# Kernel tuning notes

Measured on AMD Instinct MI355X. Metric: run time of the kernel, lower is better.

## Reference

```python
import jax, jax.numpy as jnp
import numpy as np

RADIUS = 1.3
COARSE = 64
FINE = 2
N_ATOMS = 64
SH_DIM = 9
DATA_DIM = SH_DIM * 3 + 1  # 28
N_INTRS = COARSE * 3 * 2 * FINE  # 768
STEP = (RADIUS * 2.0 / COARSE / FINE) / 2.0
BATCH = 1024


def sh_basis(d):
    # real spherical harmonics basis, degree 2 (9 coeffs), on normalized dirs
    d = d / jnp.linalg.norm(d, axis=-1, keepdims=True)
    x, y, z = d[..., 0], d[..., 1], d[..., 2]
    C0 = 0.28209479177387814
    C1 = 0.4886025119029199
    C20, C21, C22, C23, C24 = (1.0925484305920792, -1.0925484305920792,
                               0.31539156525252005, -1.0925484305920792,
                               0.5462742152960396)
    return jnp.stack([
        C0 * jnp.ones_like(x), -C1 * y, C1 * z, -C1 * x,
        C20 * x * y, C21 * y * z, C22 * (2.0 * z * z - x * x - y * y),
        C23 * x * z, C24 * (x * x - y * y)
    ], axis=-1)


def dict_interp(grid, atoms, pts):
    # l2_interp_v2: coarse-voxel dictionary coeffs x trilinear fine-atom interp
    # pts: [P,3] in [0,1)
    P = pts.shape[0]
    pc = pts * COARSE
    c = jnp.clip(jnp.floor(pc), 0, COARSE - 1).astype(jnp.int32)
    local = pc - c.astype(pts.dtype)  # position inside coarse voxel, [0,1)
    clin = (c[:, 0] * COARSE + c[:, 1]) * COARSE + c[:, 2]
    coeff = grid[clin]                              # [P, A]
    # project dictionary coeffs through atoms for every fine cell: [P, FINE^3, D]
    proj = jnp.einsum('pa,fad->pfd', coeff, atoms)
    u = local * FINE - 0.5
    f = jnp.floor(u)
    t = u - f
    i0 = jnp.clip(f, 0, FINE - 1).astype(jnp.int32)
    i1 = jnp.clip(f + 1.0, 0, FINE - 1).astype(jnp.int32)
    idx = jnp.stack([i0, i1], axis=-1)              # [P,3,2]
    w = jnp.stack([1.0 - t, t], axis=-1)            # [P,3,2]
    rows = jnp.arange(P)
    out = jnp.zeros((P, DATA_DIM), dtype=pts.dtype)
    for kx in (0, 1):
        for ky in (0, 1):
            for kz in (0, 1):
                lin = (idx[:, 0, kx] * FINE + idx[:, 1, ky]) * FINE + idx[:, 2, kz]
                wgt = w[:, 0, kx] * w[:, 1, ky] * w[:, 2, kz]
                out = out + wgt[:, None] * proj[rows, lin]
    return out


def _forward(rays_o, rays_d, grid, atoms):
    dt = rays_o.dtype
    # ---- sample_proposal (no grad) ----
    off_pos = (RADIUS - rays_o) / rays_d
    off_neg = (-RADIUS - rays_o) / rays_d
    start = jnp.max(jnp.minimum(off_pos, off_neg), axis=-1, keepdims=True)
    intersections = jax.lax.stop_gradient(
        start + jnp.arange(N_INTRS, dtype=dt)[None, :] * STEP)  # [B, 768]
    tr = intersections[:, :-1]  # [B, 767]
    pts = rays_o[:, None, :] + tr[..., None] * rays_d[:, None, :]  # [B,n,3]
    mask = jnp.all((pts > -RADIUS) & (pts < RADIUS), axis=-1)      # [B,n]
    pts = jax.lax.stop_gradient(pts)
    B, n = tr.shape
    # normalized coords in [0,1); masked-out points are clipped then zeroed later
    p = jnp.clip((pts + RADIUS) / (2.0 * RADIUS), 0.0, 1.0 - 1e-6).reshape(-1, 3)
    data = dict_interp(grid, atoms, p).reshape(B, n, DATA_DIM)
    # masked_scatter of sigma <=> dense compute + where(mask, ., 0)
    sigma = jnp.where(mask, jax.nn.relu(data[..., -1]), 0.0)
    dists = (intersections[:, 1:] - intersections[:, :-1]) * \
        jnp.linalg.norm(rays_d, axis=-1, keepdims=True)
    alpha = 1.0 - jnp.exp(-sigma * dists)
    trans = jnp.cumprod(1.0 - alpha + 1e-10, axis=-1)
    trans = jnp.concatenate([jnp.ones_like(trans[:, :1]), trans[:, :-1]], axis=-1)
    abs_light = alpha * trans  # per-sample weights
    sh_mult = sh_basis(rays_d)                      # [B, 9]
    sh = data[..., :-1].reshape(B, n, 3, SH_DIM)
    rgb_samp = jnp.einsum('bnck,bk->bnc', sh, sh_mult)
    rgb_samp = jax.nn.sigmoid(jnp.where(mask[..., None], rgb_samp, 0.0))
    comp = jnp.sum(abs_light[..., None] * rgb_samp, axis=1)  # [B,3]
    acc = jnp.sum(abs_light, axis=1)
    rgb = comp + (1.0 - acc)[:, None]  # white background
    depth = jnp.sum(abs_light * tr, axis=1)
    return rgb, alpha, depth


def setup_inputs():
    key = jax.random.key(0)
    k0, k1, k2, k3 = jax.random.split(key, 4)
    o = jax.random.normal(k0, (BATCH, 3), dtype=jnp.float32)
    o = o / jnp.linalg.norm(o, axis=-1, keepdims=True) * 2.5
    d = -o + 0.3 * jax.random.normal(k1, (BATCH, 3), dtype=jnp.float32)
    d = d / jnp.linalg.norm(d, axis=-1, keepdims=True)
    grid = 0.01 * jax.random.normal(k2, (COARSE ** 3, N_ATOMS), dtype=jnp.float32)
    atoms_sh = jax.random.uniform(k3, (FINE ** 3, N_ATOMS, DATA_DIM - 1), dtype=jnp.float32)
    atoms = jnp.concatenate(
        [atoms_sh, jnp.full((FINE ** 3, N_ATOMS, 1), 0.01, dtype=jnp.float32)], axis=-1)
    return {"rays_o": o, "rays_d": d, "grid": grid, "atoms": atoms, "grid_id": 0}


def reference(rays_o, rays_d, grid, atoms, grid_id):
    # grid_id selects among num_scenes grids; num_scenes=1 so grid is pre-selected
    return _forward(rays_o, rays_d, grid, atoms)
```

## Files before the change

### kernel.cpp

```cpp
#include <hip/hip_runtime.h>
#include <hip/hip_bf16.h>

#define RADIUS_F 1.3f
#define NSAMP 767
#define STEPF 0.01015625f
#define BATCH 1024

typedef __attribute__((ext_vector_type(8))) short short8;
typedef __attribute__((ext_vector_type(4))) float floatx4;

static __device__ __forceinline__ unsigned pkbf(float a, float b) {
    union { __hip_bfloat162 h; unsigned u; } cvt;
    cvt.h = __float22bfloat162_rn(make_float2(a, b));
    return cvt.u;
}

static __device__ __forceinline__ float coset4_sum(float p) {
    int q4 = __builtin_amdgcn_update_dpp(0, __float_as_int(p), 0x124, 0xf, 0xf, true);
    p = p + __int_as_float(q4);
    int q8 = __builtin_amdgcn_update_dpp(0, __float_as_int(p), 0x128, 0xf, 0xf, true);
    return p + __int_as_float(q8);
}

__launch_bounds__(256, 2)
__global__ void plenoxels_fwd(const float* __restrict__ rays_o,
                              const float* __restrict__ rays_d,
                              const float* __restrict__ grid,
                              const float* __restrict__ atoms,
                              float* __restrict__ out)
{
    __shared__ __align__(16) __hip_bfloat16 BpL[32 * 64];
    __shared__ __align__(16) float WL[4][16 * 12];
    __shared__ __align__(16) __hip_bfloat16 alphaL[768];
    __shared__ __align__(16) __hip_bfloat16 rgbL[768 * 3];

    const int tid  = threadIdx.x;
    const int ray  = blockIdx.x;
    const int lane = tid & 63;
    const int w    = tid >> 6;
    const int m    = lane & 15;
    const int quad = lane >> 4;

    const float ox = rays_o[ray * 3 + 0], oy = rays_o[ray * 3 + 1], oz = rays_o[ray * 3 + 2];
    const float dx = rays_d[ray * 3 + 0], dy = rays_d[ray * 3 + 1], dz = rays_d[ray * 3 + 2];

    float start;
    {
        float a0 = (RADIUS_F - ox) / dx, b0 = (-RADIUS_F - ox) / dx;
        float a1 = (RADIUS_F - oy) / dy, b1 = (-RADIUS_F - oy) / dy;
        float a2 = (RADIUS_F - oz) / dz, b2 = (-RADIUS_F - oz) / dz;
        start = fmaxf(fminf(a0, b0), fmaxf(fminf(a1, b1), fminf(a2, b2)));
    }
    const float dnorm = sqrtf(dx * dx + dy * dy + dz * dz);
    const float dist = STEPF * dnorm;

    float shm[9];
    {
        float inv = 1.0f / dnorm;
        float nx = dx * inv, ny = dy * inv, nz = dz * inv;
        shm[0] = 0.28209479177387814f;
        shm[1] = -0.4886025119029199f * ny;
        shm[2] = 0.4886025119029199f * nz;
        shm[3] = -0.4886025119029199f * nx;
        shm[4] = 1.0925484305920792f * nx * ny;
        shm[5] = -1.0925484305920792f * ny * nz;
        shm[6] = 0.31539156525252005f * (2.f * nz * nz - nx * nx - ny * ny);
        shm[7] = -1.0925484305920792f * nx * nz;
        shm[8] = 0.5462742152960396f * (nx * nx - ny * ny);
    }

    for (int idx = tid; idx < 2048; idx += 256) {
        int col = idx >> 6, a = idx & 63;
        int f = col >> 2, c = col & 3;
        const float* base = atoms + (f * 64 + a) * 28;
        float sv;
        if (c == 3) sv = base[27];
        else {
            sv = 0.f;
            #pragma unroll
            for (int i = 0; i < 9; ++i) sv = fmaf(base[c * 9 + i], shm[i], sv);
        }
        BpL[col * 64 + a] = __float2bfloat16(sv);
    }
    __syncthreads();

    short8 bq00, bq01, bq10, bq11;
    {
        const short* bs = (const short*)BpL;
        const short* p0 = bs + m * 64 + (quad << 4);
        bq00 = *(const short8*)(p0);
        bq01 = *(const short8*)(p0 + 8);
        const short* p1 = bs + (16 + m) * 64 + (quad << 4);
        bq10 = *(const short8*)(p1);
        bq11 = *(const short8*)(p1 + 8);
    }

    float* out_rgb   = out;
    float* out_alpha = out + BATCH * 3;
    float* out_depth = out + BATCH * 3 + BATCH * NSAMP;
    const float4* g4 = (const float4*)grid;

    auto geom = [&](int s, float4& WA, float4& WB, int& clin) {
        float tr = start + (float)s * STEPF;
        float px = ox + tr * dx, py = oy + tr * dy, pz = oz + tr * dz;
        int mask = (px > -RADIUS_F) & (px < RADIUS_F) &
                   (py > -RADIUS_F) & (py < RADIUS_F) &
                   (pz > -RADIUS_F) & (pz < RADIUS_F);
        float maskf = mask ? 1.f : 0.f;
        const float sc = 1.0f / (2.0f * RADIUS_F);
        float qx = fminf(fmaxf((px + RADIUS_F) * sc, 0.f), 1.0f - 1e-6f);
        float qy = fminf(fmaxf((py + RADIUS_F) * sc, 0.f), 1.0f - 1e-6f);
        float qz = fminf(fmaxf((pz + RADIUS_F) * sc, 0.f), 1.0f - 1e-6f);
        float pcx = qx * 64.f, pcy = qy * 64.f, pcz = qz * 64.f;
        float cx = fminf(floorf(pcx), 63.f);
        float cy = fminf(floorf(pcy), 63.f);
        float cz = fminf(floorf(pcz), 63.f);
        float lx = pcx - cx, ly = pcy - cy, lz = pcz - cz;
        clin = (((int)cx * 64) + (int)cy) * 64 + (int)cz;
        float xw0, xw1, yw0, yw1, zw0, zw1;
        {
            float u = lx * 2.f - 0.5f, fF = floorf(u), t = u - fF;
            xw0 = (fF < 0.f) ? 1.f : ((fF > 0.f) ? 0.f : 1.f - t);
            xw1 = (fF < 0.f) ? 0.f : ((fF > 0.f) ? 1.f : t);
        }
        {
            float u = ly * 2.f - 0.5f, fF = floorf(u), t = u - fF;
            yw0 = (fF < 0.f) ? 1.f : ((fF > 0.f) ? 0.f : 1.f - t);
            yw1 = (fF < 0.f) ? 0.f : ((fF > 0.f) ? 1.f : t);
        }
        {
            float u = lz * 2.f - 0.5f, fF = floorf(u), t = u - fF;
            zw0 = (fF < 0.f) ? 1.f : ((fF > 0.f) ? 0.f : 1.f - t);
            zw1 = (fF < 0.f) ? 0.f : ((fF > 0.f) ? 1.f : t);
        }
        xw0 *= maskf; xw1 *= maskf;
        WA = make_float4(xw0 * yw0 * zw0, xw0 * yw0 * zw1, xw0 * yw1 * zw0, xw0 * yw1 * zw1);
        WB = make_float4(xw1 * yw0 * zw0, xw1 * yw0 * zw1, xw1 * yw1 * zw0, xw1 * yw1 * zw1);
    };

    float4 WAc, WBc; int clinC;
    geom(w * 192 + m, WAc, WBc, clinC);
    float4 cv0, cv1, cv2, cv3;
    {
        const float4* gp = g4 + (clinC << 4) + (quad << 2);
        cv0 = gp[0]; cv1 = gp[1]; cv2 = gp[2]; cv3 = gp[3];
    }

    for (int t = 0; t < 12; ++t) {
        const int tile = w * 12 + t;

        if (quad == 0) {
            float* wrow = &WL[w][m * 12];
            *(float4*)(wrow)     = WAc;
            *(float4*)(wrow + 4) = WBc;
        }

        union { unsigned u[4]; short8 s; } a0, a1;
        a0.u[0] = pkbf(cv0.x, cv0.y); a0.u[1] = pkbf(cv0.z, cv0.w);
        a0.u[2] = pkbf(cv1.x, cv1.y); a0.u[3] = pkbf(cv1.z, cv1.w);
        a1.u[0] = pkbf(cv2.x, cv2.y); a1.u[1] = pkbf(cv2.z, cv2.w);
        a1.u[2] = pkbf(cv3.x, cv3.y); a1.u[3] = pkbf(cv3.z, cv3.w);

        if (t < 11) {
            geom(w * 192 + (t + 1) * 16 + m, WAc, WBc, clinC);
            const float4* gp = g4 + (clinC << 4) + (quad << 2);
            cv0 = gp[0]; cv1 = gp[1]; cv2 = gp[2]; cv3 = gp[3];
        }

        floatx4 acc0 = {0.f, 0.f, 0.f, 0.f};
        floatx4 acc1 = {0.f, 0.f, 0.f, 0.f};
        acc0 = __builtin_amdgcn_mfma_f32_16x16x32_bf16(a0.s, bq00, acc0, 0, 0, 0);
        acc0 = __builtin_amdgcn_mfma_f32_16x16x32_bf16(a1.s, bq01, acc0, 0, 0, 0);
        acc1 = __builtin_amdgcn_mfma_f32_16x16x32_bf16(a0.s, bq10, acc1, 0, 0, 0);
        acc1 = __builtin_amdgcn_mfma_f32_16x16x32_bf16(a1.s, bq11, acc1, 0, 0, 0);

        const int f0 = m >> 2;
        #pragma unroll
        for (int r = 0; r < 4; ++r) {
            const float* wrow = &WL[w][((quad << 2) + r) * 12];
            float wA = wrow[f0];
            float wB = wrow[4 + f0];
            float p = wA * acc0[r] + wB * acc1[r];
            p = coset4_sum(p);
            int s = (tile << 4) + (quad << 2) + r;
            if (s < NSAMP) {
                if (m == 3) {
                    float al = 1.f - __expf(-fmaxf(p, 0.f) * dist);
                    out_alpha[ray * NSAMP + s] = al;
                    alphaL[s] = __float2bfloat16(al);
                } else if (m < 3) {
                    rgbL[s * 3 + m] = __float2bfloat16(1.f / (1.f + __expf(-p)));
                }
            }
        }
    }

    __syncthreads();

    if (tid < 64) {
        int sA = tid * 12;
        int sB = min(sA + 12, NSAMP);
        float prod = 1.f;
        for (int s = sA; s < sB; ++s)
            prod *= (1.f - __bfloat162float(alphaL[s]) + 1e-10f);

        float incl = prod;
        #pragma unroll
        for (int off = 1; off < 64; off <<= 1) {
            float v = __shfl_up(incl, off, 64);
            if (tid >= off) incl *= v;
        }
        float excl = __shfl_up(incl, 1, 64);
        if (tid == 0) excl = 1.f;

        float trans = excl;
        float c0 = 0.f, c1 = 0.f, c2 = 0.f, acc = 0.f, dep = 0.f;
        for (int s = sA; s < sB; ++s) {
            float a = __bfloat162float(alphaL[s]);
            float wgt = a * trans;
            c0 += wgt * __bfloat162float(rgbL[s * 3 + 0]);
            c1 += wgt * __bfloat162float(rgbL[s * 3 + 1]);
            c2 += wgt * __bfloat162float(rgbL[s * 3 + 2]);
            acc += wgt;
            dep += wgt * (start + (float)s * STEPF);
            trans *= (1.f - a + 1e-10f);
        }
        #pragma unroll
        for (int off = 1; off < 64; off <<= 1) {
            c0  += __shfl_xor(c0, off, 64);
            c1  += __shfl_xor(c1, off, 64);
            c2  += __shfl_xor(c2, off, 64);
            acc += __shfl_xor(acc, off, 64);
            dep += __shfl_xor(dep, off, 64);
        }
        if (tid == 0) {
            float bg = 1.f - acc;
            out_rgb[ray * 3 + 0] = c0 + bg;
            out_rgb[ray * 3 + 1] = c1 + bg;
            out_rgb[ray * 3 + 2] = c2 + bg;
            out_depth[ray] = dep;
        }
    }
}

extern "C" void kernel_launch(void* const* d_in, const int* in_sizes, int n_in,
                              void* d_out, int out_size, void* d_ws, size_t ws_size,
                              hipStream_t stream) {
    const float* rays_o = (const float*)d_in[0];
    const float* rays_d = (const float*)d_in[1];
    const float* grid   = (const float*)d_in[2];
    const float* atoms  = (const float*)d_in[3];
    float* out = (float*)d_out;
    hipLaunchKernelGGL(plenoxels_fwd, dim3(BATCH), dim3(256), 0, stream,
                       rays_o, rays_d, grid, atoms, out);
}
```

Before: 124.4 us.

## Split ray march into per-segment sample kernel and separate compositing kernel

Splits the single per-ray kernel into two launches. The first handles a third of each ray's samples per block, giving three times as many blocks with higher occupancy bounds. It computes all geometry up front into shared tables instead of prefetching it per tile, and writes packed bf16 rgb/alpha to workspace. The second kernel does the transmittance scan and reduction with one wave per ray. The cost is that every block recomputes the atom projection, there is a workspace round-trip, and there is an extra launch.

```diff
diff --git a/kernel.cpp b/kernel.cpp
--- a/kernel.cpp
+++ b/kernel.cpp
@@ -13,6 +13,16 @@
     union { __hip_bfloat162 h; unsigned u; } cvt;
     cvt.h = __float22bfloat162_rn(make_float2(a, b));
     return cvt.u;
+}
+static __device__ __forceinline__ unsigned short bf16bits(float a) {
+    union { __hip_bfloat16 h; unsigned short u; } cvt;
+    cvt.h = __float2bfloat16(a);
+    return cvt.u;
+}
+static __device__ __forceinline__ float frombits(unsigned short u) {
+    union { unsigned short u; __hip_bfloat16 h; } cvt;
+    cvt.u = u;
+    return __bfloat162float(cvt.h);
 }
 
 static __device__ __forceinline__ float coset4_sum(float p) {
@@ -22,22 +32,27 @@
     return p + __int_as_float(q8);
 }
 
-__launch_bounds__(256, 2)
-__global__ void plenoxels_fwd(const float* __restrict__ rays_o,
-                              const float* __restrict__ rays_d,
-                              const float* __restrict__ grid,
-                              const float* __restrict__ atoms,
-                              float* __restrict__ out)
+__launch_bounds__(256, 4)
+__global__ void plen_samples(const float* __restrict__ rays_o,
+                             const float* __restrict__ rays_d,
+                             const float* __restrict__ grid,
+                             const float* __restrict__ atoms,
+                             float* __restrict__ out_alpha,
+                             uint2* __restrict__ pack)
 {
     __shared__ __align__(16) __hip_bfloat16 BpL[32 * 64];
-    __shared__ __align__(16) float WL[4][16 * 12];
-    __shared__ __align__(16) __hip_bfloat16 alphaL[768];
-    __shared__ __align__(16) __hip_bfloat16 rgbL[768 * 3];
+    __shared__ float Wf[4][8][65];
+    __shared__ int clinT[4][64];
+    __shared__ __align__(16) uint2 packT[4][64];
 
     const int tid  = threadIdx.x;
-    const int ray  = blockIdx.x;
+    const int bid  = blockIdx.x;
+    const int ray  = bid / 3;
+    const int seg  = bid - ray * 3;
     const int lane = tid & 63;
     const int w    = tid >> 6;
+    const int job  = seg * 4 + w;
+    const int sbase = job * 64;
     const int m    = lane & 15;
     const int quad = lane >> 4;
 
@@ -69,38 +84,8 @@
         shm[8] = 0.5462742152960396f * (nx * nx - ny * ny);
     }
 
-    for (int idx = tid; idx < 2048; idx += 256) {
-        int col = idx >> 6, a = idx & 63;
-        int f = col >> 2, c = col & 3;
-        const float* base = atoms + (f * 64 + a) * 28;
-        float sv;
-        if (c == 3) sv = base[27];
-        else {
-            sv = 0.f;
-            #pragma unroll
-            for (int i = 0; i < 9; ++i) sv = fmaf(base[c * 9 + i], shm[i], sv);
-        }
-        BpL[col * 64 + a] = __float2bfloat16(sv);
-    }
-    __syncthreads();
-
-    short8 bq00, bq01, bq10, bq11;
-    {
-        const short* bs = (const short*)BpL;
-        const short* p0 = bs + m * 64 + (quad << 4);
-        bq00 = *(const short8*)(p0);
-        bq01 = *(const short8*)(p0 + 8);
-        const short* p1 = bs + (16 + m) * 64 + (quad << 4);
-        bq10 = *(const short8*)(p1);
-        bq11 = *(const short8*)(p1 + 8);
-    }
-
-    float* out_rgb   = out;
-    float* out_alpha = out + BATCH * 3;
-    float* out_depth = out + BATCH * 3 + BATCH * NSAMP;
-    const float4* g4 = (const float4*)grid;
-
-    auto geom = [&](int s, float4& WA, float4& WB, int& clin) {
+    {
+        const int s = sbase + lane;
         float tr = start + (float)s * STEPF;
         float px = ox + tr * dx, py = oy + tr * dy, pz = oz + tr * dz;
         int mask = (px > -RADIUS_F) & (px < RADIUS_F) &
@@ -116,7 +101,7 @@
         float cy = fminf(floorf(pcy), 63.f);
         float cz = fminf(floorf(pcz), 63.f);
         float lx = pcx - cx, ly = pcy - cy, lz = pcz - cz;
-        clin = (((int)cx * 64) + (int)cy) * 64 + (int)cz;
+        int clin = (((int)cx * 64) + (int)cy) * 64 + (int)cz;
         float xw0, xw1, yw0, yw1, zw0, zw1;
         {
             float u = lx * 2.f - 0.5f, fF = floorf(u), t = u - fF;
@@ -134,35 +119,63 @@
             zw1 = (fF < 0.f) ? 0.f : ((fF > 0.f) ? 1.f : t);
         }
         xw0 *= maskf; xw1 *= maskf;
-        WA = make_float4(xw0 * yw0 * zw0, xw0 * yw0 * zw1, xw0 * yw1 * zw0, xw0 * yw1 * zw1);
-        WB = make_float4(xw1 * yw0 * zw0, xw1 * yw0 * zw1, xw1 * yw1 * zw0, xw1 * yw1 * zw1);
-    };
-
-    float4 WAc, WBc; int clinC;
-    geom(w * 192 + m, WAc, WBc, clinC);
+        Wf[w][0][lane] = xw0 * yw0 * zw0;
+        Wf[w][1][lane] = xw0 * yw0 * zw1;
+        Wf[w][2][lane] = xw0 * yw1 * zw0;
+        Wf[w][3][lane] = xw0 * yw1 * zw1;
+        Wf[w][4][lane] = xw1 * yw0 * zw0;
+        Wf[w][5][lane] = xw1 * yw0 * zw1;
+        Wf[w][6][lane] = xw1 * yw1 * zw0;
+        Wf[w][7][lane] = xw1 * yw1 * zw1;
+        clinT[w][lane] = clin;
+    }
+
+    const float4* g4 = (const float4*)grid;
     float4 cv0, cv1, cv2, cv3;
     {
+        int clinC = clinT[w][m];
         const float4* gp = g4 + (clinC << 4) + (quad << 2);
         cv0 = gp[0]; cv1 = gp[1]; cv2 = gp[2]; cv3 = gp[3];
     }
 
-    for (int t = 0; t < 12; ++t) {
-        const int tile = w * 12 + t;
-
-        if (quad == 0) {
-            float* wrow = &WL[w][m * 12];
-            *(float4*)(wrow)     = WAc;
-            *(float4*)(wrow + 4) = WBc;
-        }
-
+    for (int idx = tid; idx < 2048; idx += 256) {
+        int col = idx >> 6, a = idx & 63;
+        int f = col >> 2, c = col & 3;
+        const float* base = atoms + (f * 64 + a) * 28;
+        float sv;
+        if (c == 3) sv = base[27];
+        else {
+            sv = 0.f;
+            #pragma unroll
+            for (int i = 0; i < 9; ++i) sv = fmaf(base[c * 9 + i], shm[i], sv);
+        }
+        BpL[col * 64 + a] = __float2bfloat16(sv);
+    }
+    __syncthreads();
+
+    short8 bq00, bq01, bq10, bq11;
+    {
+        const short* bs = (const short*)BpL;
+        const short* p0 = bs + m * 64 + (quad << 4);
+        bq00 = *(const short8*)(p0);
+        bq01 = *(const short8*)(p0 + 8);
+        const short* p1 = bs + (16 + m) * 64 + (quad << 4);
+        bq10 = *(const short8*)(p1);
+        bq11 = *(const short8*)(p1 + 8);
+    }
+
+    unsigned short* ps = (unsigned short*)packT;
+    const int f0 = m >> 2;
+
+    for (int t = 0; t < 4; ++t) {
         union { unsigned u[4]; short8 s; } a0, a1;
         a0.u[0] = pkbf(cv0.x, cv0.y); a0.u[1] = pkbf(cv0.z, cv0.w);
         a0.u[2] = pkbf(cv1.x, cv1.y); a0.u[3] = pkbf(cv1.z, cv1.w);
         a1.u[0] = pkbf(cv2.x, cv2.y); a1.u[1] = pkbf(cv2.z, cv2.w);
         a1.u[2] = pkbf(cv3.x, cv3.y); a1.u[3] = pkbf(cv3.z, cv3.w);
 
-        if (t < 11) {
-            geom(w * 192 + (t + 1) * 16 + m, WAc, WBc, clinC);
+        if (t < 3) {
+            int clinC = clinT[w][((t + 1) << 4) + m];
             const float4* gp = g4 + (clinC << 4) + (quad << 2);
             cv0 = gp[0]; cv1 = gp[1]; cv2 = gp[2]; cv3 = gp[3];
         }
@@ -174,72 +187,103 @@
         acc1 = __builtin_amdgcn_mfma_f32_16x16x32_bf16(a0.s, bq10, acc1, 0, 0, 0);
         acc1 = __builtin_amdgcn_mfma_f32_16x16x32_bf16(a1.s, bq11, acc1, 0, 0, 0);
 
-        const int f0 = m >> 2;
         #pragma unroll
         for (int r = 0; r < 4; ++r) {
-            const float* wrow = &WL[w][((quad << 2) + r) * 12];
-            float wA = wrow[f0];
-            float wB = wrow[4 + f0];
+            int sl = (t << 4) + (quad << 2) + r;
+            float wA = Wf[w][f0][sl];
+            float wB = Wf[w][4 + f0][sl];
             float p = wA * acc0[r] + wB * acc1[r];
             p = coset4_sum(p);
-            int s = (tile << 4) + (quad << 2) + r;
-            if (s < NSAMP) {
-                if (m == 3) {
-                    float al = 1.f - __expf(-fmaxf(p, 0.f) * dist);
-                    out_alpha[ray * NSAMP + s] = al;
-                    alphaL[s] = __float2bfloat16(al);
-                } else if (m < 3) {
-                    rgbL[s * 3 + m] = __float2bfloat16(1.f / (1.f + __expf(-p)));
-                }
+            float val;
+            if (m == 3) {
+                val = 1.f - __expf(-fmaxf(p, 0.f) * dist);
+                int s = sbase + sl;
+                if (s < NSAMP) out_alpha[ray * NSAMP + s] = val;
+            } else {
+                val = 1.f / (1.f + __expf(-p));
             }
-        }
-    }
-
-    __syncthreads();
-
-    if (tid < 64) {
-        int sA = tid * 12;
-        int sB = min(sA + 12, NSAMP);
-        float prod = 1.f;
-        for (int s = sA; s < sB; ++s)
-            prod *= (1.f - __bfloat162float(alphaL[s]) + 1e-10f);
-
-        float incl = prod;
-        #pragma unroll
-        for (int off = 1; off < 64; off <<= 1) {
-            float v = __shfl_up(incl, off, 64);
-            if (tid >= off) incl *= v;
-        }
-        float excl = __shfl_up(incl, 1, 64);
-        if (tid == 0) excl = 1.f;
-
-        float trans = excl;
-        float c0 = 0.f, c1 = 0.f, c2 = 0.f, acc = 0.f, dep = 0.f;
-        for (int s = sA; s < sB; ++s) {
-            float a = __bfloat162float(alphaL[s]);
-            float wgt = a * trans;
-            c0 += wgt * __bfloat162float(rgbL[s * 3 + 0]);
-            c1 += wgt * __bfloat162float(rgbL[s * 3 + 1]);
-            c2 += wgt * __bfloat162float(rgbL[s * 3 + 2]);
-            acc += wgt;
-            dep += wgt * (start + (float)s * STEPF);
-            trans *= (1.f - a + 1e-10f);
-        }
-        #pragma unroll
-        for (int off = 1; off < 64; off <<= 1) {
-            c0  += __shfl_xor(c0, off, 64);
-            c1  += __shfl_xor(c1, off, 64);
-            c2  += __shfl_xor(c2, off, 64);
-            acc += __shfl_xor(acc, off, 64);
-            dep += __shfl_xor(dep, off, 64);
-        }
-        if (tid == 0) {
-            float bg = 1.f - acc;
-            out_rgb[ray * 3 + 0] = c0 + bg;
-            out_rgb[ray * 3 + 1] = c1 + bg;
-            out_rgb[ray * 3 + 2] = c2 + bg;
-            out_depth[ray] = dep;
-        }
+            if (m < 4) ps[(((w << 6) + sl) << 2) + m] = bf16bits(val);
+        }
+    }
+
+    uint2 pk = packT[w][lane];
+    pack[ray * 768 + sbase + lane] = pk;
+}
+
+__launch_bounds__(256, 2)
+__global__ void plen_composite(const float* __restrict__ rays_o,
+                               const float* __restrict__ rays_d,
+                               const uint2* __restrict__ pack,
+                               float* __restrict__ out)
+{
+    const int tid  = threadIdx.x;
+    const int lane = tid & 63;
+    const int w    = tid >> 6;
+    const int ray  = blockIdx.x * 4 + w;
+
+    const float ox = rays_o[ray * 3 + 0], oy = rays_o[ray * 3 + 1], oz = rays_o[ray * 3 + 2];
+    const float dx = rays_d[ray * 3 + 0], dy = rays_d[ray * 3 + 1], dz = rays_d[ray * 3 + 2];
+    float start;
+    {
+        float a0 = (RADIUS_F - ox) / dx, b0 = (-RADIUS_F - ox) / dx;
+        float a1 = (RADIUS_F - oy) / dy, b1 = (-RADIUS_F - oy) / dy;
+        float a2 = (RADIUS_F - oz) / dz, b2 = (-RADIUS_F - oz) / dz;
+        start = fmaxf(fminf(a0, b0), fmaxf(fminf(a1, b1), fminf(a2, b2)));
+    }
+
+    float* out_rgb   = out;
+    float* out_depth = out + BATCH * 3 + BATCH * NSAMP;
+
+    const int sA = lane * 12;
+    const int sB = min(sA + 12, NSAMP);
+    const uint2* pr = pack + ray * 768 + sA;
+
+    uint2 e[12];
+    #pragma unroll
+    for (int i = 0; i < 12; ++i) e[i] = pr[i];
+
+    float prod = 1.f;
+    for (int s = sA; s < sB; ++s) {
+        float a = frombits((unsigned short)(e[s - sA].y >> 16));
+        prod *= (1.f - a + 1e-10f);
+    }
+
+    float incl = prod;
+    #pragma unroll
+    for (int off = 1; off < 64; off <<= 1) {
+        float v = __shfl_up(incl, off, 64);
+        if (lane >= off) incl *= v;
+    }
+    float excl = __shfl_up(incl, 1, 64);
+    if (lane == 0) excl = 1.f;
+
+    float trans = excl;
+    float c0 = 0.f, c1 = 0.f, c2 = 0.f, acc = 0.f, dep = 0.f;
+    for (int s = sA; s < sB; ++s) {
+        uint2 ev = e[s - sA];
+        float a  = frombits((unsigned short)(ev.y >> 16));
+        float wgt = a * trans;
+        c0 += wgt * frombits((unsigned short)(ev.x & 0xffff));
+        c1 += wgt * frombits((unsigned short)(ev.x >> 16));
+        c2 += wgt * frombits((unsigned short)(ev.y & 0xffff));
+        acc += wgt;
+        dep += wgt * (start + (float)s * STEPF);
+        trans *= (1.f - a + 1e-10f);
+    }
+    #pragma unroll
+    for (int off = 1; off < 64; off <<= 1) {
+        c0  += __shfl_xor(c0, off, 64);
+        c1  += __shfl_xor(c1, off, 64);
+        c2  += __shfl_xor(c2, off, 64);
+        acc += __shfl_xor(acc, off, 64);
+        dep += __shfl_xor(dep, off, 64);
+    }
+    if (lane == 0) {
+        float bg = 1.f - acc;
+        out_rgb[ray * 3 + 0] = c0 + bg;
+        out_rgb[ray * 3 + 1] = c1 + bg;
+        out_rgb[ray * 3 + 2] = c2 + bg;
+        out_depth[ray] = dep;
     }
 }
 
@@ -250,7 +294,11 @@
     const float* rays_d = (const float*)d_in[1];
     const float* grid   = (const float*)d_in[2];
     const float* atoms  = (const float*)d_in[3];
-    float* out = (float*)d_out;
-    hipLaunchKernelGGL(plenoxels_fwd, dim3(BATCH), dim3(256), 0, stream,
-                       rays_o, rays_d, grid, atoms, out);
-}
+    float* out  = (float*)d_out;
+    uint2* pack = (uint2*)d_ws;
+
+    hipLaunchKernelGGL(plen_samples, dim3(BATCH * 3), dim3(256), 0, stream,
+                       rays_o, rays_d, grid, atoms, out + BATCH * 3, pack);
+    hipLaunchKernelGGL(plen_composite, dim3(BATCH / 4), dim3(256), 0, stream,
+                       rays_o, rays_d, pack, out);
+}
```

Result: slower. 134.0 us (+7.8%).
